# Kernel optimization log

Measured on AMD Instinct MI355X. Metric: run time of the kernel, lower is better.

Reference implementation:

```python
import jax, jax.numpy as jnp
import numpy as np

N_SPECIES = 4  # species ids 0..3


def setup_inputs() -> dict:
    key = jax.random.key(0)
    k1, k2, k3, k4 = jax.random.split(key, 4)
    NTA, O, NMAX = 65536, 512, 512
    rho = jax.random.normal(k1, (NTA, O), dtype=jnp.float32)
    # per-species expert Linear(O -> NMAX): weights stacked [S, O, NMAX], bias [S, NMAX]
    W = jax.random.normal(k2, (N_SPECIES, O, NMAX), dtype=jnp.float32) * (1.0 / np.sqrt(O))
    b = jax.random.normal(k3, (N_SPECIES, NMAX), dtype=jnp.float32) * 0.01
    symbols = jax.random.randint(k4, (NTA,), 0, N_SPECIES, dtype=jnp.int32)
    return {"rho": rho, "W": W, "b": b, "symbols": symbols}


def reference(rho, W, b, symbols):
    # Faithful to Gj.forward: coeff[mask] = expert_spe(rho[mask]) for each species.
    # Vectorized form: apply each species' Linear to all atoms (dense GEMM),
    # then select per-atom by species mask. Loop is over the small fixed
    # species set (4), not over data dims.
    NTA = rho.shape[0]
    nmax = W.shape[-1]
    coeff = jnp.zeros((NTA, nmax), dtype=rho.dtype)
    for spe in range(W.shape[0]):
        y = rho @ W[spe] + b[spe]            # [NTA, nmax]
        mask = (symbols == spe)[:, None]      # [NTA, 1]
        coeff = jnp.where(mask, y, coeff)
    return coeff
```

## Files before the change

kernel.cpp:

```cpp
#include <hip/hip_runtime.h>


#define NTA   65536
#define DIM_O 512
#define NMAXD 512
#define NSPE  4

typedef __attribute__((ext_vector_type(4))) float  f32x4;
typedef __attribute__((ext_vector_type(8))) short  bf16x8;
typedef __attribute__((ext_vector_type(4))) short  bf16x4;

__device__ __forceinline__ short f2bf(float f) {
    unsigned u = __builtin_bit_cast(unsigned, f);
    u += 0x7FFFu + ((u >> 16) & 1u);
    return (short)(u >> 16);
}

__device__ __forceinline__ void bar_lds() {
    asm volatile("s_waitcnt lgkmcnt(0)" ::: "memory");
    __builtin_amdgcn_s_barrier();
    __builtin_amdgcn_sched_barrier(0);
}

__global__ void build_lists_kernel(const int* __restrict__ sym,
                                   int* __restrict__ counts,
                                   int* __restrict__ lists) {
    int i = blockIdx.x * 256 + threadIdx.x;
    int s = sym[i];
    int lane = threadIdx.x & 63;
    #pragma unroll
    for (int spe = 0; spe < NSPE; ++spe) {
        unsigned long long m = __ballot(s == spe);
        if (m == 0ull) continue;
        int leader = __ffsll(m) - 1;
        int base = 0;
        if (lane == leader) base = atomicAdd(&counts[spe], __popcll(m));
        base = __shfl(base, leader);
        if (s == spe) {
            int pos = __popcll(m & ((1ull << lane) - 1ull));
            lists[spe * NTA + base + pos] = i;
        }
    }
}

__global__ void pack_w_kernel(const float* __restrict__ W, short* __restrict__ Wp,
                              int* __restrict__ counts) {
    if (blockIdx.x == 0 && threadIdx.x < NSPE) counts[threadIdx.x] = 0;
    int idx = blockIdx.x * 256 + threadIdx.x;
    int j  = idx & 7;
    int l  = (idx >> 3) & 63;
    int nb = (idx >> 9) & 31;
    int kb = (idx >> 14) & 15;
    int s  = idx >> 18;
    int k = kb * 32 + (l >> 4) * 8 + j;
    int n = nb * 16 + (l & 15);
    Wp[idx] = f2bf(W[((size_t)s * DIM_O + k) * NMAXD + n]);
}

__global__ __launch_bounds__(512, 2)
void gemm_kernel(const float* __restrict__ rho,
                 const short* __restrict__ Wp,
                 const float* __restrict__ bias,
                 const int*  __restrict__ counts,
                 const int*  __restrict__ lists,
                 float* __restrict__ out)
{
    const int b   = blockIdx.x;
    const int tid = threadIdx.x;
    const int lane = tid & 63;
    const int w    = tid >> 6;
    const int lrow = lane & 15;
    const int lgr  = lane >> 4;

    const int c0x = counts[0], c1x = counts[1], c2x = counts[2], c3x = counts[3];
    const int P1 = (c0x + 63) >> 6;
    const int P2 = P1 + ((c1x + 63) >> 6);
    const int P3 = P2 + ((c2x + 63) >> 6);
    const int ntot = P3 + ((c3x + 63) >> 6);

    __shared__ int aidxA[2][64];
    __shared__ __align__(16) short Abuf[64 * 64 * 8];

    const int srow  = tid >> 3;
    const int scol8 = tid & 7;
    const int cc0   = scol8 >> 1;
    const int roww  = srow ^ ((cc0 & 3) << 1);
    const int dof   = (scol8 & 1) * 4;

    #define TILE_INFO(ti, s_, mb_, cnt_)                                   \
        {   s_ = ((ti) >= P1) + ((ti) >= P2) + ((ti) >= P3);               \
            mb_ = (ti) - (s_ == 0 ? 0 : s_ == 1 ? P1 : s_ == 2 ? P2 : P3); \
            cnt_ = (s_ == 0 ? c0x : s_ == 1 ? c1x : s_ == 2 ? c2x : c3x); }

    f32x4 st[16];

    {
        int s, mb, cnt; TILE_INFO(b, s, mb, cnt);
        if (tid < 64) aidxA[0][tid] = lists[s * NTA + min(mb * 64 + tid, cnt - 1)];
    }
    __syncthreads();
    {
        const float* g = rho + (size_t)aidxA[0][srow] * DIM_O + scol8 * 4;
        #pragma unroll
        for (int r = 0; r < 16; ++r) st[r] = *(const f32x4*)(g + r * 32);
    }

    int p = 0;
    for (int ti = b; ti < ntot; ti += 256, p ^= 1) {
        int s, mb, cnt; TILE_INFO(ti, s, mb, cnt);
        const int rows_here = min(64, cnt - mb * 64);

        bar_lds();

        #pragma unroll
        for (int r = 0; r < 16; ++r) {
            bf16x4 a;
            #pragma unroll
            for (int q = 0; q < 4; ++q) a[q] = f2bf(st[r][q]);
            *(bf16x4*)&Abuf[((r * 4 + cc0) * 64 + roww) * 8 + dof] = a;
        }

        const int tn = ti + 256;
        if (tn < ntot) {
            int s2, mb2, cnt2; TILE_INFO(tn, s2, mb2, cnt2);
            if (tid < 64)
                aidxA[p ^ 1][tid] = lists[s2 * NTA + min(mb2 * 64 + tid, cnt2 - 1)];
        }
        bar_lds();

        if (tn < ntot) {
            const float* g = rho + (size_t)aidxA[p ^ 1][srow] * DIM_O + scol8 * 4;
            #pragma unroll
            for (int r = 0; r < 16; ++r) st[r] = *(const f32x4*)(g + r * 32);
        }

        const short* wbase = Wp + ((size_t)s * 512 + w * 4) * 512 + lane * 8;

        f32x4 acc[4][4];
        #pragma unroll
        for (int m = 0; m < 4; ++m)
            #pragma unroll
            for (int n = 0; n < 4; ++n) acc[m][n] = (f32x4)0.0f;

        #pragma unroll
        for (int kt = 0; kt < 8; ++kt) {
            bf16x8 bfr[2][4];
            #pragma unroll
            for (int ks = 0; ks < 2; ++ks)
                #pragma unroll
                for (int nf = 0; nf < 4; ++nf)
                    bfr[ks][nf] = *(const bf16x8*)
                        (wbase + (size_t)((kt * 2 + ks) * 32 + nf) * 512);
            #pragma unroll
            for (int ks = 0; ks < 2; ++ks) {
                #pragma unroll
                for (int mf = 0; mf < 4; ++mf) {
                    const int c = kt * 8 + ks * 4 + lgr;
                    const int r = (mf * 16 + lrow) ^ ((lgr & 3) << 1);
                    const bf16x8 afrag = *(const bf16x8*)&Abuf[(c * 64 + r) * 8];
                    #pragma unroll
                    for (int nf = 0; nf < 4; ++nf)
                        acc[mf][nf] = __builtin_amdgcn_mfma_f32_16x16x32_bf16(
                            afrag, bfr[ks][nf], acc[mf][nf], 0, 0, 0);
                }
            }
        }

        float bv[4];
        #pragma unroll
        for (int nf = 0; nf < 4; ++nf)
            bv[nf] = bias[s * NMAXD + w * 64 + nf * 16 + lrow];
        #pragma unroll
        for (int mf = 0; mf < 4; ++mf) {
            #pragma unroll
            for (int q = 0; q < 4; ++q) {
                const int r = mf * 16 + lgr * 4 + q;
                if (r < rows_here) {
                    float* orow = out + (size_t)aidxA[p][r] * NMAXD + w * 64 + lrow;
                    #pragma unroll
                    for (int nf = 0; nf < 4; ++nf)
                        orow[nf * 16] = acc[mf][nf][q] + bv[nf];
                }
            }
        }
    }
    #undef TILE_INFO
}

extern "C" void kernel_launch(void* const* d_in, const int* in_sizes, int n_in,
                              void* d_out, int out_size, void* d_ws, size_t ws_size,
                              hipStream_t stream) {
    const float* rho = (const float*)d_in[0];
    const float* W   = (const float*)d_in[1];
    const float* b   = (const float*)d_in[2];
    const int*   sym = (const int*)d_in[3];
    float* out = (float*)d_out;

    int*   counts = (int*)d_ws;
    int*   lists  = (int*)((char*)d_ws + 1024);
    short* Wp     = (short*)((char*)d_ws + 1024 + (size_t)NSPE * NTA * 4);

    pack_w_kernel<<<(NSPE * DIM_O * NMAXD) / 256, 256, 0, stream>>>(W, Wp, counts);
    build_lists_kernel<<<NTA / 256, 256, 0, stream>>>(sym, counts, lists);
    gemm_kernel<<<256, 512, 0, stream>>>(rho, Wp, b, counts, lists, out);
}
```

Before: 134.4 us.

## Warp-specialize GEMM: dedicated producer waves gather rho into double-buffered LDS

Adds 4 producer waves per block (768 threads) that gather and convert the next tile's rho rows into a second LDS buffer while the 8 consumer waves run MFMAs on the current buffer. This replaces the earlier register-staged prefetch, in which the same waves did both the gather and the compute. The aim is to overlap gather latency with compute and free consumer registers. In exchange LDS use doubles to about 128KB per block, which may cut occupancy to one block per CU. Producer waves also hold 16 float4 values each, so register pressure stays high under launch bounds of (768,3).

```diff
diff --git a/kernel.cpp b/kernel.cpp
--- a/kernel.cpp
+++ b/kernel.cpp
@@ -57,7 +57,7 @@
     Wp[idx] = f2bf(W[((size_t)s * DIM_O + k) * NMAXD + n]);
 }
 
-__global__ __launch_bounds__(512, 2)
+__global__ __launch_bounds__(768, 3)
 void gemm_kernel(const float* __restrict__ rho,
                  const short* __restrict__ Wp,
                  const float* __restrict__ bias,
@@ -65,125 +65,123 @@
                  const int*  __restrict__ lists,
                  float* __restrict__ out)
 {
-    const int b   = blockIdx.x;
-    const int tid = threadIdx.x;
+    const int b    = blockIdx.x;
+    const int tid  = threadIdx.x;
     const int lane = tid & 63;
     const int w    = tid >> 6;
-    const int lrow = lane & 15;
-    const int lgr  = lane >> 4;
 
     const int c0x = counts[0], c1x = counts[1], c2x = counts[2], c3x = counts[3];
     const int P1 = (c0x + 63) >> 6;
     const int P2 = P1 + ((c1x + 63) >> 6);
     const int P3 = P2 + ((c2x + 63) >> 6);
     const int ntot = P3 + ((c3x + 63) >> 6);
-
-    __shared__ int aidxA[2][64];
-    __shared__ __align__(16) short Abuf[64 * 64 * 8];
-
-    const int srow  = tid >> 3;
-    const int scol8 = tid & 7;
-    const int cc0   = scol8 >> 1;
-    const int roww  = srow ^ ((cc0 & 3) << 1);
-    const int dof   = (scol8 & 1) * 4;
+    if (b >= ntot) return;
+
+    __shared__ int aidx[2][64];
+    __shared__ __align__(16) short Abuf[2][64 * 64 * 8];
 
     #define TILE_INFO(ti, s_, mb_, cnt_)                                   \
         {   s_ = ((ti) >= P1) + ((ti) >= P2) + ((ti) >= P3);               \
             mb_ = (ti) - (s_ == 0 ? 0 : s_ == 1 ? P1 : s_ == 2 ? P2 : P3); \
             cnt_ = (s_ == 0 ? c0x : s_ == 1 ? c1x : s_ == 2 ? c2x : c3x); }
 
-    f32x4 st[16];
-
-    {
-        int s, mb, cnt; TILE_INFO(b, s, mb, cnt);
-        if (tid < 64) aidxA[0][tid] = lists[s * NTA + min(mb * 64 + tid, cnt - 1)];
-    }
-    __syncthreads();
-    {
-        const float* g = rho + (size_t)aidxA[0][srow] * DIM_O + scol8 * 4;
-        #pragma unroll
-        for (int r = 0; r < 16; ++r) st[r] = *(const f32x4*)(g + r * 32);
-    }
+    const int pt    = tid - 512;
+    const int scol8 = pt & 7;
+    const int cc0   = scol8 >> 1;
+    const int dof   = (scol8 & 1) * 4;
+
+    #define GATHER(ti_, dstp_)                                              \
+        {   int s2, mb2, cnt2; TILE_INFO(ti_, s2, mb2, cnt2);               \
+            if (w == 8)                                                     \
+                aidx[dstp_][lane] =                                         \
+                    lists[s2 * NTA + min(mb2 * 64 + lane, cnt2 - 1)];       \
+            _Pragma("unroll")                                               \
+            for (int ps = 0; ps < 2; ++ps) {                                \
+                const int srow = (pt >> 3) + ps * 32;                       \
+                const int gi = lists[s2 * NTA + min(mb2 * 64 + srow, cnt2 - 1)]; \
+                const float* g = rho + (size_t)gi * DIM_O + scol8 * 4;      \
+                f32x4 v[16];                                                \
+                _Pragma("unroll")                                           \
+                for (int r = 0; r < 16; ++r) v[r] = *(const f32x4*)(g + r * 32); \
+                const int roww = srow ^ ((cc0 & 3) << 1);                   \
+                short* dstb = Abuf[dstp_];                                  \
+                _Pragma("unroll")                                           \
+                for (int r = 0; r < 16; ++r) {                              \
+                    bf16x4 a;                                               \
+                    _Pragma("unroll")                                       \
+                    for (int q = 0; q < 4; ++q) a[q] = f2bf(v[r][q]);       \
+                    *(bf16x4*)&dstb[((r * 4 + cc0) * 64 + roww) * 8 + dof] = a; \
+                }                                                           \
+            }                                                               \
+        }
+
+    if (w >= 8) GATHER(b, 0);
+    bar_lds();
 
     int p = 0;
     for (int ti = b; ti < ntot; ti += 256, p ^= 1) {
-        int s, mb, cnt; TILE_INFO(ti, s, mb, cnt);
-        const int rows_here = min(64, cnt - mb * 64);
-
-        bar_lds();
-
-        #pragma unroll
-        for (int r = 0; r < 16; ++r) {
-            bf16x4 a;
-            #pragma unroll
-            for (int q = 0; q < 4; ++q) a[q] = f2bf(st[r][q]);
-            *(bf16x4*)&Abuf[((r * 4 + cc0) * 64 + roww) * 8 + dof] = a;
-        }
-
-        const int tn = ti + 256;
-        if (tn < ntot) {
-            int s2, mb2, cnt2; TILE_INFO(tn, s2, mb2, cnt2);
-            if (tid < 64)
-                aidxA[p ^ 1][tid] = lists[s2 * NTA + min(mb2 * 64 + tid, cnt2 - 1)];
+        if (w < 8) {
+            int s, mb, cnt; TILE_INFO(ti, s, mb, cnt);
+            const int rows_here = min(64, cnt - mb * 64);
+            const int lrow = lane & 15;
+            const int lgr  = lane >> 4;
+            const short* Ab = Abuf[p];
+            const short* wbase = Wp + ((size_t)s * 512 + w * 4) * 512 + lane * 8;
+
+            f32x4 acc[4][4];
+            #pragma unroll
+            for (int m = 0; m < 4; ++m)
+                #pragma unroll
+                for (int n = 0; n < 4; ++n) acc[m][n] = (f32x4)0.0f;
+
+            #pragma unroll
+            for (int kt = 0; kt < 8; ++kt) {
+                bf16x8 bfr[2][4];
+                #pragma unroll
+                for (int ks = 0; ks < 2; ++ks)
+                    #pragma unroll
+                    for (int nf = 0; nf < 4; ++nf)
+                        bfr[ks][nf] = *(const bf16x8*)
+                            (wbase + (size_t)((kt * 2 + ks) * 32 + nf) * 512);
+                #pragma unroll
+                for (int ks = 0; ks < 2; ++ks) {
+                    #pragma unroll
+                    for (int mf = 0; mf < 4; ++mf) {
+                        const int c = kt * 8 + ks * 4 + lgr;
+                        const int r = (mf * 16 + lrow) ^ ((lgr & 3) << 1);
+                        const bf16x8 afrag = *(const bf16x8*)&Ab[(c * 64 + r) * 8];
+                        #pragma unroll
+                        for (int nf = 0; nf < 4; ++nf)
+                            acc[mf][nf] = __builtin_amdgcn_mfma_f32_16x16x32_bf16(
+                                afrag, bfr[ks][nf], acc[mf][nf], 0, 0, 0);
+                    }
+                }
+            }
+
+            float bv[4];
+            #pragma unroll
+            for (int nf = 0; nf < 4; ++nf)
+                bv[nf] = bias[s * NMAXD + w * 64 + nf * 16 + lrow];
+            #pragma unroll
+            for (int mf = 0; mf < 4; ++mf) {
+                #pragma unroll
+                for (int q = 0; q < 4; ++q) {
+                    const int r = mf * 16 + lgr * 4 + q;
+                    if (r < rows_here) {
+                        float* orow = out + (size_t)aidx[p][r] * NMAXD + w * 64 + lrow;
+                        #pragma unroll
+                        for (int nf = 0; nf < 4; ++nf)
+                            orow[nf * 16] = acc[mf][nf][q] + bv[nf];
+                    }
+                }
+            }
+        } else {
+            const int tn = ti + 256;
+            if (tn < ntot) GATHER(tn, p ^ 1);
         }
         bar_lds();
-
-        if (tn < ntot) {
-            const float* g = rho + (size_t)aidxA[p ^ 1][srow] * DIM_O + scol8 * 4;
-            #pragma unroll
-            for (int r = 0; r < 16; ++r) st[r] = *(const f32x4*)(g + r * 32);
-        }
-
-        const short* wbase = Wp + ((size_t)s * 512 + w * 4) * 512 + lane * 8;
-
-        f32x4 acc[4][4];
-        #pragma unroll
-        for (int m = 0; m < 4; ++m)
-            #pragma unroll
-            for (int n = 0; n < 4; ++n) acc[m][n] = (f32x4)0.0f;
-
-        #pragma unroll
-        for (int kt = 0; kt < 8; ++kt) {
-            bf16x8 bfr[2][4];
-            #pragma unroll
-            for (int ks = 0; ks < 2; ++ks)
-                #pragma unroll
-                for (int nf = 0; nf < 4; ++nf)
-                    bfr[ks][nf] = *(const bf16x8*)
-                        (wbase + (size_t)((kt * 2 + ks) * 32 + nf) * 512);
-            #pragma unroll
-            for (int ks = 0; ks < 2; ++ks) {
-                #pragma unroll
-                for (int mf = 0; mf < 4; ++mf) {
-                    const int c = kt * 8 + ks * 4 + lgr;
-                    const int r = (mf * 16 + lrow) ^ ((lgr & 3) << 1);
-                    const bf16x8 afrag = *(const bf16x8*)&Abuf[(c * 64 + r) * 8];
-                    #pragma unroll
-                    for (int nf = 0; nf < 4; ++nf)
-                        acc[mf][nf] = __builtin_amdgcn_mfma_f32_16x16x32_bf16(
-                            afrag, bfr[ks][nf], acc[mf][nf], 0, 0, 0);
-                }
-            }
-        }
-
-        float bv[4];
-        #pragma unroll
-        for (int nf = 0; nf < 4; ++nf)
-            bv[nf] = bias[s * NMAXD + w * 64 + nf * 16 + lrow];
-        #pragma unroll
-        for (int mf = 0; mf < 4; ++mf) {
-            #pragma unroll
-            for (int q = 0; q < 4; ++q) {
-                const int r = mf * 16 + lgr * 4 + q;
-                if (r < rows_here) {
-                    float* orow = out + (size_t)aidxA[p][r] * NMAXD + w * 64 + lrow;
-                    #pragma unroll
-                    for (int nf = 0; nf < 4; ++nf)
-                        orow[nf * 16] = acc[mf][nf][q] + bv[nf];
-                }
-            }
-        }
     }
+    #undef GATHER
     #undef TILE_INFO
 }
 
@@ -202,5 +200,5 @@
 
     pack_w_kernel<<<(NSPE * DIM_O * NMAXD) / 256, 256, 0, stream>>>(W, Wp, counts);
     build_lists_kernel<<<NTA / 256, 256, 0, stream>>>(sym, counts, lists);
-    gemm_kernel<<<256, 512, 0, stream>>>(rho, Wp, b, counts, lists, out);
-}
+    gemm_kernel<<<256, 768, 0, stream>>>(rho, Wp, b, counts, lists, out);
+}
```

Result: faster. 129.0 us (-4.0%).
